# Optimization experiments

Hardware: AMD Instinct MI355X
Metric: run time of the kernel (lower is better)

## Reference

```python
import jax, jax.numpy as jnp
import numpy as np

T, B, I, H, NH = 256, 8, 1024, 1024, 16
DH = H // NH
LN_EPS = 1e-5


def setup_inputs() -> dict:
    key = jax.random.key(0)
    ks = jax.random.split(key, 8)
    def w(k, shape, fan_in):
        return jax.random.normal(k, shape, jnp.float32) / np.float32(np.sqrt(fan_in))
    inputs = jax.random.normal(ks[0], (T, B, I), jnp.float32)
    # 4 HybridGates (forget, input, update, output) stacked: Linear(I+H -> H)
    W_gates = w(ks[1], (4, H, I + H), I + H)
    b_gates = jnp.zeros((4, H), jnp.float32)
    ln_g = jnp.ones((4, H), jnp.float32)   # LayerNorm weight per gate
    ln_b = jnp.zeros((4, H), jnp.float32)  # LayerNorm bias per gate
    # MultiheadAttention in_proj (split into q/k/v) and out_proj
    Wq = w(ks[2], (H, H), H); Wk = w(ks[3], (H, H), H); Wv = w(ks[4], (H, H), H)
    bq = jnp.zeros((H,), jnp.float32); bk = jnp.zeros((H,), jnp.float32); bv = jnp.zeros((H,), jnp.float32)
    Wo = w(ks[5], (H, H), H); bo = jnp.zeros((H,), jnp.float32)
    return dict(inputs=inputs, W_gates=W_gates, b_gates=b_gates, ln_g=ln_g, ln_b=ln_b,
                Wq=Wq, Wk=Wk, Wv=Wv, bq=bq, bk=bk, bv=bv, Wo=Wo, bo=bo)


def _layernorm(x, g, b):
    m = jnp.mean(x, axis=-1, keepdims=True)
    v = jnp.var(x, axis=-1, keepdims=True)
    return (x - m) * jax.lax.rsqrt(v + LN_EPS) * g + b


def reference(inputs, W_gates, b_gates, ln_g, ln_b, Wq, Wk, Wv, bq, bk, bv, Wo, bo):
    Tn, Bn, _ = inputs.shape
    scale = 1.0 / np.float32(np.sqrt(DH))
    pos = jnp.arange(Tn)

    def step(carry, x_t):
        hx, cx, Kb, Vb, t = carry  # Kb/Vb: [T, B, NH, DH] cached projections of past outputs
        combined = jnp.concatenate([x_t, hx], axis=1)          # [B, I+H]
        z = jnp.einsum('bd,khd->kbh', combined, W_gates) + b_gates[:, None, :]
        z = _layernorm(z, ln_g[:, None, :], ln_b[:, None, :])  # [4, B, H]
        f = jax.nn.sigmoid(z[0]); i = jax.nn.sigmoid(z[1])
        g = jnp.tanh(z[2]);       o = jax.nn.sigmoid(z[3])
        cx = f * cx + i * g
        h0 = o * jnp.tanh(cx)                                   # [B, H]
        # attention of current hidden over all previously produced outputs
        q = (h0 @ Wq.T + bq).reshape(Bn, NH, DH)
        scores = jnp.einsum('bhd,sbhd->bhs', q, Kb) * scale     # [B, NH, T]
        scores = jnp.where((pos < t)[None, None, :], scores, -1e9)
        attn = jax.nn.softmax(scores, axis=-1)
        ctx = jnp.einsum('bhs,sbhd->bhd', attn, Vb).reshape(Bn, H)
        attn_out = ctx @ Wo.T + bo
        hx = h0 + jnp.where(t > 0, attn_out, 0.0)               # no attention at t=0
        # cache k/v projections of the new output (linear, so per-token projection is exact)
        Kb = Kb.at[t].set((hx @ Wk.T + bk).reshape(Bn, NH, DH))
        Vb = Vb.at[t].set((hx @ Wv.T + bv).reshape(Bn, NH, DH))
        return (hx, cx, Kb, Vb, t + 1), hx

    init = (jnp.zeros((Bn, H), inputs.dtype), jnp.zeros((Bn, H), inputs.dtype),
            jnp.zeros((Tn, Bn, NH, DH), inputs.dtype), jnp.zeros((Tn, Bn, NH, DH), inputs.dtype),
            jnp.int32(0))
    (hx, cx, _, _, _), outputs = jax.lax.scan(step, init, inputs)
    return outputs, hx, cx
```

## Files before the change

kernel.cpp:

```cpp
#include <hip/hip_runtime.h>
#include <math.h>

#define NBLK 256
#define NTHR 512
#define GATHER 255

#define OFF_HX    0
#define OFF_H0    8192
#define OFF_CTX   16384
#define OFF_Z     24576
#define OFF_KB    57344
#define OFF_VB    (OFF_KB + 2097152)
#define OFF_FLAGS (OFF_VB + 2097152)
#define FLG_U32   (4096 + 128)

#define S_WG    0
#define S_STAGE 32768
#define S_CX    36864
#define S_H0L   37888
#define S_Q     38912
#define S_PS    38976
#define S_RED   39232
#define S_R2    39248
#define S_EH    39264
#define S_ZX    39296
#define S_KVX   39424
#define LDS_FLOATS 39488
#define LDS_BYTES  (LDS_FLOATS * 4)

typedef unsigned long long u64;
union F2U { u64 u; float2 f; };

__device__ __forceinline__ float ld1(const float* p) {
    return __hip_atomic_load(const_cast<float*>(p), __ATOMIC_RELAXED, __HIP_MEMORY_SCOPE_AGENT);
}
__device__ __forceinline__ void st1(float* p, float v) {
    __hip_atomic_store(p, v, __ATOMIC_RELAXED, __HIP_MEMORY_SCOPE_AGENT);
}
__device__ __forceinline__ unsigned ldu(const unsigned* p) {
    return __hip_atomic_load(const_cast<unsigned*>(p), __ATOMIC_RELAXED, __HIP_MEMORY_SCOPE_AGENT);
}
__device__ __forceinline__ void stu(unsigned* p, unsigned v) {
    __hip_atomic_store(p, v, __ATOMIC_RELAXED, __HIP_MEMORY_SCOPE_AGENT);
}
__device__ __forceinline__ float2 ld2(const float* p) {
    F2U c; c.u = __hip_atomic_load(reinterpret_cast<u64*>(const_cast<float*>(p)),
                                   __ATOMIC_RELAXED, __HIP_MEMORY_SCOPE_AGENT);
    return c.f;
}
__device__ __forceinline__ float4 ld4(const float* p) {
    float2 a = ld2(p), b = ld2(p + 2);
    return make_float4(a.x, a.y, b.x, b.y);
}
__device__ __forceinline__ float dot4(const float4 a, const float4 b) {
    return a.x*b.x + a.y*b.y + a.z*b.z + a.w*b.w;
}

__device__ __forceinline__ void arrive(unsigned* flags, int blk, unsigned bc) {
    __syncthreads();
    if (threadIdx.x == 0) stu(flags + blk * 16, bc);
}
__device__ __forceinline__ void waitbar(unsigned* flags, unsigned* golines,
                                        unsigned bc, int blk) {
    if (blk == GATHER) {
        if (threadIdx.x < 256)
            while (ldu(flags + threadIdx.x * 16) < bc) __builtin_amdgcn_s_sleep(4);
        __syncthreads();
        if (threadIdx.x < 8) stu(golines + threadIdx.x * 16, bc);
    } else {
        if (threadIdx.x == 0)
            while (ldu(golines + (blk >> 5) * 16) < bc) __builtin_amdgcn_s_sleep(4);
    }
    __syncthreads();
}

__global__ __launch_bounds__(NTHR, 1)
void qlstm_kernel(const float* __restrict__ x,  const float* __restrict__ Wg,
                  const float* __restrict__ bg, const float* __restrict__ lng,
                  const float* __restrict__ lnb,const float* __restrict__ Wq,
                  const float* __restrict__ Wk, const float* __restrict__ Wv,
                  const float* __restrict__ bq, const float* __restrict__ bk,
                  const float* __restrict__ bv, const float* __restrict__ Wo,
                  const float* __restrict__ bo, float* __restrict__ out,
                  float* __restrict__ ws)
{
    extern __shared__ float lds[];
    const int blk = blockIdx.x, tid = threadIdx.x;
    const int w = tid >> 6, l = tid & 63;

    float* hx  = ws + OFF_HX;   float* h0g = ws + OFF_H0;
    float* ctx = ws + OFF_CTX;  float* z   = ws + OFF_Z;
    float* Kb  = ws + OFF_KB;   float* Vb  = ws + OFF_VB;
    unsigned* flags   = (unsigned*)(ws + OFF_FLAGS);
    unsigned* golines = flags + 4096;
    unsigned bc = 1;

    {
        const float* wsrc = Wg + (size_t)blk * 32768;
        #pragma unroll
        for (int j = 0; j < 16; ++j) {
            const int fi = j * 512 + tid;
            *(float4*)(lds + S_WG + fi * 4) = *(const float4*)(wsrc + fi * 4);
        }
    }
    const int kv_mat = blk >> 7;
    const int kv_h   = (blk & 127) * 8 + w;
    const float* kv_wrow = (kv_mat ? Wv : Wk) + (size_t)kv_h * 1024;
    float4 wkv[4];
    #pragma unroll
    for (int i = 0; i < 4; ++i) wkv[i] = *(const float4*)(kv_wrow + i * 256 + l * 4);
    const float kv_bias = (kv_mat ? bv : bk)[kv_h];
    const int g     = blk >> 6;
    const int hbase = (blk & 63) * 16;
    const int h0r   = hbase + 2 * w;
    const float bg0 = bg[g * 1024 + h0r], bg1 = bg[g * 1024 + h0r + 1];
    float lnw0[4], lnw1[4], lnb0[4], lnb1[4];
    #pragma unroll
    for (int g2 = 0; g2 < 4; ++g2) {
        lnw0[g2] = lng[g2 * 1024 + tid];       lnb0[g2] = lnb[g2 * 1024 + tid];
        lnw1[g2] = lng[g2 * 1024 + 512 + tid]; lnb1[g2] = lnb[g2 * 1024 + 512 + tid];
    }
    const float bo0 = bo[blk*4+0], bo1 = bo[blk*4+1], bo2 = bo[blk*4+2], bo3 = bo[blk*4+3];
    const int ab = blk >> 4, anh = blk & 15;
    const bool h0_writer = (blk < 128) && ((blk & 15) == 0);
    const int qdh = tid >> 3, qks = tid & 7;
    const float q_bias = (blk < 128) ? bq[anh * 64 + qdh] : 0.f;

    { const int gi = blk * NTHR + tid; if (gi < 8192) st1(hx + gi, 0.f); }
    if (tid < 256) *(float4*)(lds + S_CX + tid * 4) = make_float4(0,0,0,0);
    arrive(flags, blk, bc);

    for (int t = 0; t < 256; ++t) {
        float a0[8], a1[8];
        {
            const float* xt = x + (size_t)t * 8192;
            #pragma unroll
            for (int b = 0; b < 8; ++b) { a0[b] = 0.f; a1[b] = 0.f; }
            #pragma unroll
            for (int i = 0; i < 4; ++i) {
                const int k = i * 256 + l * 4;
                const float4 w0 = *(const float4*)(lds + S_WG + (2*w)   * 2048 + k);
                const float4 w1 = *(const float4*)(lds + S_WG + (2*w+1) * 2048 + k);
                #pragma unroll
                for (int b = 0; b < 8; ++b) {
                    const float4 a = *(const float4*)(xt + b * 1024 + k);
                    a0[b] += dot4(w0, a); a1[b] += dot4(w1, a);
                }
            }
        }
        waitbar(flags, golines, bc, blk);

        {
            float akv[8];
            #pragma unroll
            for (int b = 0; b < 8; ++b) akv[b] = 0.f;
            float2 hreg[8];
            #pragma unroll
            for (int c = 0; c < 2; ++c)
                #pragma unroll
                for (int j = 0; j < 4; ++j) {
                    const int idx = j * 512 + tid;
                    const int b = idx >> 8, off2 = idx & 255;
                    hreg[c * 4 + j] = ld2(hx + b * 1024 + c * 512 + off2 * 2);
                }
            #pragma unroll
            for (int c = 0; c < 2; ++c) {
                if (c) __syncthreads();
                #pragma unroll
                for (int j = 0; j < 4; ++j)
                    *(float2*)(lds + S_STAGE + (j * 512 + tid) * 2) = hreg[c * 4 + j];
                __syncthreads();
                #pragma unroll
                for (int ii = 0; ii < 2; ++ii) {
                    const int k = ii * 256 + l * 4;
                    const float4 w0 = *(const float4*)(lds + S_WG + (2*w)   * 2048 + 1024 + c * 512 + k);
                    const float4 w1 = *(const float4*)(lds + S_WG + (2*w+1) * 2048 + 1024 + c * 512 + k);
                    const float4 wk = wkv[c * 2 + ii];
                    #pragma unroll
                    for (int b = 0; b < 8; ++b) {
                        const float4 a = *(const float4*)(lds + S_STAGE + b * 512 + k);
                        a0[b] += dot4(w0, a); a1[b] += dot4(w1, a); akv[b] += dot4(wk, a);
                    }
                }
            }
            #pragma unroll
            for (int o = 1; o < 64; o <<= 1)
                #pragma unroll
                for (int b = 0; b < 8; ++b) {
                    a0[b]  += __shfl_xor(a0[b], o);
                    a1[b]  += __shfl_xor(a1[b], o);
                    akv[b] += __shfl_xor(akv[b], o);
                }
            if (l == 0) {
                #pragma unroll
                for (int b = 0; b < 8; ++b) {
                    lds[S_ZX + (2*w)   * 8 + b] = a0[b] + bg0;
                    lds[S_ZX + (2*w+1) * 8 + b] = a1[b] + bg1;
                    lds[S_KVX + w * 8 + b]      = akv[b] + kv_bias;
                }
            }
            __syncthreads();
            if (tid < 128) {
                const int h = tid & 15, b2 = tid >> 4;
                st1(z + (size_t)(g * 8 + b2) * 1024 + hbase + h, lds[S_ZX + h * 8 + b2]);
            } else if (tid < 192 && t > 0) {
                const int j = tid - 128;
                const int b2 = j >> 3, hh = j & 7;
                float* dst = kv_mat ? Vb : Kb;
                st1(dst + ((size_t)(t - 1) * 8 + b2) * 1024 + (blk & 127) * 8 + hh,
                    lds[S_KVX + hh * 8 + b2]);
            }
        }
        ++bc; arrive(flags, blk, bc);
        waitbar(flags, golines, bc, blk);

        if (blk < 128) {
            #pragma unroll
            for (int j = 0; j < 4; ++j) {
                const int idx = j * 512 + tid;
                const int g2 = idx >> 9, off2 = idx & 511;
                *(float2*)(lds + S_STAGE + idx * 2) = ld2(z + ((size_t)g2 * 8 + ab) * 1024 + off2 * 2);
            }
            __syncthreads();
            const int gt = w >> 1, hf = w & 1;
            float s = 0.f, q2s = 0.f;
            #pragma unroll
            for (int j = 0; j < 8; ++j) {
                const float v = lds[S_STAGE + gt * 1024 + hf * 512 + j * 64 + l];
                s += v; q2s += v * v;
            }
            #pragma unroll
            for (int o = 1; o < 64; o <<= 1) { s += __shfl_xor(s, o); q2s += __shfl_xor(q2s, o); }
            if (l == 0) { lds[S_RED + w] = s; lds[S_R2 + w] = q2s; }
            __syncthreads();
            float mean[4], rstd[4];
            #pragma unroll
            for (int g2 = 0; g2 < 4; ++g2) {
                const float ss = lds[S_RED + 2*g2] + lds[S_RED + 2*g2 + 1];
                const float qq = lds[S_R2  + 2*g2] + lds[S_R2  + 2*g2 + 1];
                const float m = ss * (1.f / 1024.f);
                mean[g2] = m;
                rstd[g2] = rsqrtf(qq * (1.f / 1024.f) - m * m + 1e-5f);
            }
            {
                float zv[4];
                #pragma unroll
                for (int g2 = 0; g2 < 4; ++g2)
                    zv[g2] = (lds[S_STAGE + g2 * 1024 + tid] - mean[g2]) * rstd[g2] * lnw0[g2] + lnb0[g2];
                const float f  = 1.f / (1.f + __expf(-zv[0]));
                const float ii = 1.f / (1.f + __expf(-zv[1]));
                const float gg = tanhf(zv[2]);
                const float oo = 1.f / (1.f + __expf(-zv[3]));
                const float c  = f * lds[S_CX + tid] + ii * gg;
                lds[S_CX + tid] = c;
                const float ho = oo * tanhf(c);
                lds[S_H0L + tid] = ho;
                if (h0_writer) st1(h0g + ab * 1024 + tid, ho);
            }
            {
                float zv[4];
                #pragma unroll
                for (int g2 = 0; g2 < 4; ++g2)
                    zv[g2] = (lds[S_STAGE + g2 * 1024 + 512 + tid] - mean[g2]) * rstd[g2] * lnw1[g2] + lnb1[g2];
                const float f  = 1.f / (1.f + __expf(-zv[0]));
                const float ii = 1.f / (1.f + __expf(-zv[1]));
                const float gg = tanhf(zv[2]);
                const float oo = 1.f / (1.f + __expf(-zv[3]));
                const float c  = f * lds[S_CX + 512 + tid] + ii * gg;
                lds[S_CX + 512 + tid] = c;
                const float ho = oo * tanhf(c);
                lds[S_H0L + 512 + tid] = ho;
                if (h0_writer) st1(h0g + ab * 1024 + 512 + tid, ho);
            }
            __syncthreads();
            {
                const float* wrow = Wq + (size_t)(anh * 64 + qdh) * 1024;
                float qa = 0.f;
                #pragma unroll 8
                for (int j = 0; j < 32; ++j) {
                    const int k = j * 32 + qks * 4;
                    qa += dot4(*(const float4*)(wrow + k), *(const float4*)(lds + S_H0L + k));
                }
                qa += __shfl_xor(qa, 1); qa += __shfl_xor(qa, 2); qa += __shfl_xor(qa, 4);
                if (qks == 0) lds[S_Q + qdh] = (qa + q_bias) * 0.125f;
            }
            __syncthreads();
            if (t > 0) {
                float sc = -1e30f;
                if (tid < t) {
                    const float* kr = Kb + ((size_t)tid * 8 + ab) * 1024 + anh * 64;
                    float d = 0.f;
                    #pragma unroll
                    for (int j = 0; j < 16; ++j) {
                        const float4 k4 = ld4(kr + j * 4);
                        d += k4.x*lds[S_Q + j*4]   + k4.y*lds[S_Q + j*4+1]
                           + k4.z*lds[S_Q + j*4+2] + k4.w*lds[S_Q + j*4+3];
                    }
                    sc = d;
                }
                float mx = sc;
                #pragma unroll
                for (int o = 1; o < 64; o <<= 1) mx = fmaxf(mx, __shfl_xor(mx, o));
                if (l == 0) lds[S_RED + w] = mx;
                __syncthreads();
                mx = lds[S_RED];
                #pragma unroll
                for (int j = 1; j < 8; ++j) mx = fmaxf(mx, lds[S_RED + j]);
                const float p = (tid < t) ? __expf(sc - mx) : 0.f;
                if (tid < 256) lds[S_PS + tid] = p;
                float ps = p;
                #pragma unroll
                for (int o = 1; o < 64; o <<= 1) ps += __shfl_xor(ps, o);
                if (l == 0) lds[S_R2 + w] = ps;
                __syncthreads();
                float tot = lds[S_R2];
                #pragma unroll
                for (int j = 1; j < 8; ++j) tot += lds[S_R2 + j];
                const float inv = 1.f / tot;
                const int dh2 = tid & 31, ss = tid >> 5;
                float cax = 0.f, cay = 0.f;
                for (int s2 = ss; s2 < t; s2 += 16) {
                    const float pp = lds[S_PS + s2];
                    const float2 v2 = ld2(Vb + ((size_t)s2 * 8 + ab) * 1024 + anh * 64 + dh2 * 2);
                    cax += pp * v2.x; cay += pp * v2.y;
                }
                *(float2*)(lds + S_STAGE + tid * 2) = make_float2(cax, cay);
                __syncthreads();
                if (tid < 64) {
                    float v = 0.f;
                    #pragma unroll
                    for (int j = 0; j < 16; ++j) v += lds[S_STAGE + j * 64 + tid];
                    st1(ctx + ab * 1024 + anh * 64 + tid, v * inv);
                }
            }
        }
        ++bc; arrive(flags, blk, bc);
        waitbar(flags, golines, bc, blk);

        {
            if (tid < 32)
                lds[S_EH + tid] = ld1(h0g + (size_t)(tid >> 2) * 1024 + blk * 4 + (tid & 3));
            const int b = w;
            float o0 = 0.f, o1 = 0.f, o2 = 0.f, o3 = 0.f;
            if (t > 0) {
                const float* cb = ctx + b * 1024;
                #pragma unroll
                for (int i = 0; i < 4; ++i) {
                    const int k = i * 256 + l * 4;
                    const float4 c4 = ld4(cb + k);
                    o0 += dot4(*(const float4*)(Wo + (size_t)(blk*4+0) * 1024 + k), c4);
                    o1 += dot4(*(const float4*)(Wo + (size_t)(blk*4+1) * 1024 + k), c4);
                    o2 += dot4(*(const float4*)(Wo + (size_t)(blk*4+2) * 1024 + k), c4);
                    o3 += dot4(*(const float4*)(Wo + (size_t)(blk*4+3) * 1024 + k), c4);
                }
                #pragma unroll
                for (int o = 1; o < 64; o <<= 1) {
                    o0 += __shfl_xor(o0, o); o1 += __shfl_xor(o1, o);
                    o2 += __shfl_xor(o2, o); o3 += __shfl_xor(o3, o);
                }
            }
            __syncthreads();
            if (l == 0) {
                const float v0 = (t > 0) ? lds[S_EH + w*4 + 0] + o0 + bo0 : lds[S_EH + w*4 + 0];
                const float v1 = (t > 0) ? lds[S_EH + w*4 + 1] + o1 + bo1 : lds[S_EH + w*4 + 1];
                const float v2 = (t > 0) ? lds[S_EH + w*4 + 2] + o2 + bo2 : lds[S_EH + w*4 + 2];
                const float v3 = (t > 0) ? lds[S_EH + w*4 + 3] + o3 + bo3 : lds[S_EH + w*4 + 3];
                st1(hx + b * 1024 + blk*4 + 0, v0);
                st1(hx + b * 1024 + blk*4 + 1, v1);
                st1(hx + b * 1024 + blk*4 + 2, v2);
                st1(hx + b * 1024 + blk*4 + 3, v3);
                float* op = out + (size_t)t * 8192 + b * 1024 + blk * 4;
                op[0] = v0; op[1] = v1; op[2] = v2; op[3] = v3;
            }
        }
        ++bc; arrive(flags, blk, bc);
    }
    waitbar(flags, golines, bc, blk);

    if (h0_writer) {
        out[2097152 + 8192 + ab * 1024 + tid]       = lds[S_CX + tid];
        out[2097152 + 8192 + ab * 1024 + 512 + tid] = lds[S_CX + 512 + tid];
    }
    if (blk >= 136 && blk < 144) {
        const int b = blk - 136;
        out[2097152 + b * 1024 + tid]       = ld1(hx + b * 1024 + tid);
        out[2097152 + b * 1024 + 512 + tid] = ld1(hx + b * 1024 + 512 + tid);
    }
}

extern "C" void kernel_launch(void* const* d_in, const int* in_sizes, int n_in,
                              void* d_out, int out_size, void* d_ws, size_t ws_size,
                              hipStream_t stream) {
    const float* x   = (const float*)d_in[0];
    const float* Wg  = (const float*)d_in[1];
    const float* bg  = (const float*)d_in[2];
    const float* lng = (const float*)d_in[3];
    const float* lnb = (const float*)d_in[4];
    const float* Wq  = (const float*)d_in[5];
    const float* Wk  = (const float*)d_in[6];
    const float* Wv  = (const float*)d_in[7];
    const float* bq  = (const float*)d_in[8];
    const float* bk  = (const float*)d_in[9];
    const float* bv  = (const float*)d_in[10];
    const float* Wo  = (const float*)d_in[11];
    const float* bo  = (const float*)d_in[12];
    float* out = (float*)d_out;
    float* ws  = (float*)d_ws;

    static int attr_set = 0;
    if (!attr_set) {
        hipFuncSetAttribute((const void*)qlstm_kernel,
                            hipFuncAttributeMaxDynamicSharedMemorySize, LDS_BYTES);
        attr_set = 1;
    }
    hipMemsetAsync((char*)d_ws + (size_t)OFF_FLAGS * 4, 0, (size_t)FLG_U32 * 4, stream);

    void* args[] = { &x, &Wg, &bg, &lng, &lnb, &Wq, &Wk, &Wv,
                     &bq, &bk, &bv, &Wo, &bo, &out, &ws };
    hipLaunchCooperativeKernel((void*)qlstm_kernel, dim3(NBLK), dim3(NTHR),
                               args, LDS_BYTES, stream);
}
```

Measured before the change: 11.72 ms.

## Store hidden state and K/V cache in bf16 and restructure score and out-proj mapping

Stores the broadcast hidden state and the K/V attention cache as packed bf16 instead of fp32. This halves the global traffic for the recurrent hidden-state reads and the attention cache scans. It also restructures the score computation so 16 lanes cooperate per key row with shuffle reductions, and remaps the out-projection so each block computes 2 rows by 2 batches. The cost is reduced precision in the recurrence and attention, which may push errors past tolerance, plus an extra barrier in the softmax.

```diff
diff --git a/kernel.cpp b/kernel.cpp
--- a/kernel.cpp
+++ b/kernel.cpp
@@ -6,12 +6,13 @@
 #define GATHER 255
 
 #define OFF_HX    0
-#define OFF_H0    8192
-#define OFF_CTX   16384
-#define OFF_Z     24576
-#define OFF_KB    57344
-#define OFF_VB    (OFF_KB + 2097152)
-#define OFF_FLAGS (OFF_VB + 2097152)
+#define OFF_HXH   8192
+#define OFF_H0    12288
+#define OFF_CTX   20480
+#define OFF_Z     28672
+#define OFF_KBH   61440
+#define OFF_VBH   (OFF_KBH + 1048576)
+#define OFF_FLAGS (OFF_VBH + 1048576)
 #define FLG_U32   (4096 + 128)
 
 #define S_WG    0
@@ -43,17 +44,37 @@
 __device__ __forceinline__ void stu(unsigned* p, unsigned v) {
     __hip_atomic_store(p, v, __ATOMIC_RELAXED, __HIP_MEMORY_SCOPE_AGENT);
 }
+__device__ __forceinline__ u64 ldu64(const unsigned* p) {
+    return __hip_atomic_load(reinterpret_cast<u64*>(const_cast<unsigned*>(p)),
+                             __ATOMIC_RELAXED, __HIP_MEMORY_SCOPE_AGENT);
+}
 __device__ __forceinline__ float2 ld2(const float* p) {
     F2U c; c.u = __hip_atomic_load(reinterpret_cast<u64*>(const_cast<float*>(p)),
                                    __ATOMIC_RELAXED, __HIP_MEMORY_SCOPE_AGENT);
     return c.f;
 }
+__device__ __forceinline__ void st2(float* p, float2 v) {
+    F2U c; c.f = v;
+    __hip_atomic_store(reinterpret_cast<u64*>(p), c.u,
+                       __ATOMIC_RELAXED, __HIP_MEMORY_SCOPE_AGENT);
+}
 __device__ __forceinline__ float4 ld4(const float* p) {
     float2 a = ld2(p), b = ld2(p + 2);
     return make_float4(a.x, a.y, b.x, b.y);
 }
 __device__ __forceinline__ float dot4(const float4 a, const float4 b) {
     return a.x*b.x + a.y*b.y + a.z*b.z + a.w*b.w;
+}
+__device__ __forceinline__ unsigned pack_bf16(float lo, float hi) {
+    unsigned ul = __builtin_bit_cast(unsigned, lo);
+    ul = (ul + 0x7FFFu + ((ul >> 16) & 1u)) >> 16;
+    unsigned uh = __builtin_bit_cast(unsigned, hi);
+    uh = (uh + 0x7FFFu + ((uh >> 16) & 1u)) >> 16;
+    return ul | (uh << 16);
+}
+__device__ __forceinline__ float2 unpack_bf16(unsigned u) {
+    return make_float2(__builtin_bit_cast(float, u << 16),
+                       __builtin_bit_cast(float, u & 0xFFFF0000u));
 }
 
 __device__ __forceinline__ void arrive(unsigned* flags, int blk, unsigned bc) {
@@ -88,9 +109,13 @@
     const int blk = blockIdx.x, tid = threadIdx.x;
     const int w = tid >> 6, l = tid & 63;
 
-    float* hx  = ws + OFF_HX;   float* h0g = ws + OFF_H0;
-    float* ctx = ws + OFF_CTX;  float* z   = ws + OFF_Z;
-    float* Kb  = ws + OFF_KB;   float* Vb  = ws + OFF_VB;
+    float* hx   = ws + OFF_HX;
+    unsigned* hxh = (unsigned*)(ws + OFF_HXH);
+    float* h0g  = ws + OFF_H0;
+    float* ctx  = ws + OFF_CTX;
+    float* z    = ws + OFF_Z;
+    unsigned* Kbh = (unsigned*)(ws + OFF_KBH);
+    unsigned* Vbh = (unsigned*)(ws + OFF_VBH);
     unsigned* flags   = (unsigned*)(ws + OFF_FLAGS);
     unsigned* golines = flags + 4096;
     unsigned bc = 1;
@@ -114,19 +139,27 @@
     const int hbase = (blk & 63) * 16;
     const int h0r   = hbase + 2 * w;
     const float bg0 = bg[g * 1024 + h0r], bg1 = bg[g * 1024 + h0r + 1];
-    float lnw0[4], lnw1[4], lnb0[4], lnb1[4];
+    float lnw0[4], lnw1[4], lnb0v[4], lnb1v[4];
     #pragma unroll
     for (int g2 = 0; g2 < 4; ++g2) {
-        lnw0[g2] = lng[g2 * 1024 + tid];       lnb0[g2] = lnb[g2 * 1024 + tid];
-        lnw1[g2] = lng[g2 * 1024 + 512 + tid]; lnb1[g2] = lnb[g2 * 1024 + 512 + tid];
-    }
-    const float bo0 = bo[blk*4+0], bo1 = bo[blk*4+1], bo2 = bo[blk*4+2], bo3 = bo[blk*4+3];
+        lnw0[g2] = lng[g2 * 1024 + tid];       lnb0v[g2] = lnb[g2 * 1024 + tid];
+        lnw1[g2] = lng[g2 * 1024 + 512 + tid]; lnb1v[g2] = lnb[g2 * 1024 + 512 + tid];
+    }
+    const int rg = blk >> 2, bp = blk & 3;
+    const int er0 = rg * 16 + 2 * w;
+    const int eb0 = bp * 2, eb1 = eb0 + 1;
+    const float bor0 = bo[er0], bor1 = bo[er0 + 1];
     const int ab = blk >> 4, anh = blk & 15;
     const bool h0_writer = (blk < 128) && ((blk & 15) == 0);
     const int qdh = tid >> 3, qks = tid & 7;
     const float q_bias = (blk < 128) ? bq[anh * 64 + qdh] : 0.f;
-
-    { const int gi = blk * NTHR + tid; if (gi < 8192) st1(hx + gi, 0.f); }
+    const int sr = tid >> 4, l16 = tid & 15;
+
+    {
+        const int gi = blk * NTHR + tid;
+        if (gi < 8192) st1(hx + gi, 0.f);
+        else if (gi < 12288) stu(hxh + gi - 8192, 0u);
+    }
     if (tid < 256) *(float4*)(lds + S_CX + tid * 4) = make_float4(0,0,0,0);
     arrive(flags, blk, bc);
 
@@ -154,21 +187,24 @@
             float akv[8];
             #pragma unroll
             for (int b = 0; b < 8; ++b) akv[b] = 0.f;
-            float2 hreg[8];
+            unsigned hregu[8];
             #pragma unroll
             for (int c = 0; c < 2; ++c)
                 #pragma unroll
                 for (int j = 0; j < 4; ++j) {
-                    const int idx = j * 512 + tid;
-                    const int b = idx >> 8, off2 = idx & 255;
-                    hreg[c * 4 + j] = ld2(hx + b * 1024 + c * 512 + off2 * 2);
+                    const int ix = j * 512 + tid;
+                    const int b = ix >> 8, p = ix & 255;
+                    hregu[c * 4 + j] = ldu(hxh + b * 512 + c * 256 + p);
                 }
             #pragma unroll
             for (int c = 0; c < 2; ++c) {
                 if (c) __syncthreads();
                 #pragma unroll
-                for (int j = 0; j < 4; ++j)
-                    *(float2*)(lds + S_STAGE + (j * 512 + tid) * 2) = hreg[c * 4 + j];
+                for (int j = 0; j < 4; ++j) {
+                    const int ix = j * 512 + tid;
+                    const int b = ix >> 8, p = ix & 255;
+                    *(float2*)(lds + S_STAGE + b * 512 + p * 2) = unpack_bf16(hregu[c * 4 + j]);
+                }
                 __syncthreads();
                 #pragma unroll
                 for (int ii = 0; ii < 2; ++ii) {
@@ -203,12 +239,12 @@
             if (tid < 128) {
                 const int h = tid & 15, b2 = tid >> 4;
                 st1(z + (size_t)(g * 8 + b2) * 1024 + hbase + h, lds[S_ZX + h * 8 + b2]);
-            } else if (tid < 192 && t > 0) {
+            } else if (tid < 160 && t > 0) {
                 const int j = tid - 128;
-                const int b2 = j >> 3, hh = j & 7;
-                float* dst = kv_mat ? Vb : Kb;
-                st1(dst + ((size_t)(t - 1) * 8 + b2) * 1024 + (blk & 127) * 8 + hh,
-                    lds[S_KVX + hh * 8 + b2]);
+                const int b2 = j >> 2, hp = j & 3;
+                unsigned* dst = kv_mat ? Vbh : Kbh;
+                stu(dst + ((size_t)(t - 1) * 8 + b2) * 512 + (blk & 127) * 4 + hp,
+                    pack_bf16(lds[S_KVX + (2*hp) * 8 + b2], lds[S_KVX + (2*hp+1) * 8 + b2]));
             }
         }
         ++bc; arrive(flags, blk, bc);
@@ -246,7 +282,7 @@
                 float zv[4];
                 #pragma unroll
                 for (int g2 = 0; g2 < 4; ++g2)
-                    zv[g2] = (lds[S_STAGE + g2 * 1024 + tid] - mean[g2]) * rstd[g2] * lnw0[g2] + lnb0[g2];
+                    zv[g2] = (lds[S_STAGE + g2 * 1024 + tid] - mean[g2]) * rstd[g2] * lnw0[g2] + lnb0v[g2];
                 const float f  = 1.f / (1.f + __expf(-zv[0]));
                 const float ii = 1.f / (1.f + __expf(-zv[1]));
                 const float gg = tanhf(zv[2]);
@@ -261,7 +297,7 @@
                 float zv[4];
                 #pragma unroll
                 for (int g2 = 0; g2 < 4; ++g2)
-                    zv[g2] = (lds[S_STAGE + g2 * 1024 + 512 + tid] - mean[g2]) * rstd[g2] * lnw1[g2] + lnb1[g2];
+                    zv[g2] = (lds[S_STAGE + g2 * 1024 + 512 + tid] - mean[g2]) * rstd[g2] * lnw1[g2] + lnb1v[g2];
                 const float f  = 1.f / (1.f + __expf(-zv[0]));
                 const float ii = 1.f / (1.f + __expf(-zv[1]));
                 const float gg = tanhf(zv[2]);
@@ -286,18 +322,22 @@
             }
             __syncthreads();
             if (t > 0) {
-                float sc = -1e30f;
-                if (tid < t) {
-                    const float* kr = Kb + ((size_t)tid * 8 + ab) * 1024 + anh * 64;
+                for (int s0 = 0; s0 < t; s0 += 32) {
+                    const int s2 = s0 + sr;
                     float d = 0.f;
-                    #pragma unroll
-                    for (int j = 0; j < 16; ++j) {
-                        const float4 k4 = ld4(kr + j * 4);
-                        d += k4.x*lds[S_Q + j*4]   + k4.y*lds[S_Q + j*4+1]
-                           + k4.z*lds[S_Q + j*4+2] + k4.w*lds[S_Q + j*4+3];
+                    if (s2 < t) {
+                        F2U c; c.u = ldu64(Kbh + ((size_t)s2 * 8 + ab) * 512 + anh * 32 + l16 * 2);
+                        const float2 p0 = unpack_bf16((unsigned)(c.u & 0xFFFFFFFFu));
+                        const float2 p1 = unpack_bf16((unsigned)(c.u >> 32));
+                        d = p0.x*lds[S_Q + l16*4]   + p0.y*lds[S_Q + l16*4+1]
+                          + p1.x*lds[S_Q + l16*4+2] + p1.y*lds[S_Q + l16*4+3];
                     }
-                    sc = d;
-                }
+                    d += __shfl_xor(d, 1); d += __shfl_xor(d, 2);
+                    d += __shfl_xor(d, 4); d += __shfl_xor(d, 8);
+                    if (s2 < t && l16 == 0) lds[S_PS + s2] = d;
+                }
+                __syncthreads();
+                float sc = (tid < t) ? lds[S_PS + tid] : -1e30f;
                 float mx = sc;
                 #pragma unroll
                 for (int o = 1; o < 64; o <<= 1) mx = fmaxf(mx, __shfl_xor(mx, o));
@@ -307,6 +347,7 @@
                 #pragma unroll
                 for (int j = 1; j < 8; ++j) mx = fmaxf(mx, lds[S_RED + j]);
                 const float p = (tid < t) ? __expf(sc - mx) : 0.f;
+                __syncthreads();
                 if (tid < 256) lds[S_PS + tid] = p;
                 float ps = p;
                 #pragma unroll
@@ -317,11 +358,11 @@
                 #pragma unroll
                 for (int j = 1; j < 8; ++j) tot += lds[S_R2 + j];
                 const float inv = 1.f / tot;
-                const int dh2 = tid & 31, ss = tid >> 5;
+                const int dh2 = tid & 31, ss2 = tid >> 5;
                 float cax = 0.f, cay = 0.f;
-                for (int s2 = ss; s2 < t; s2 += 16) {
+                for (int s2 = ss2; s2 < t; s2 += 16) {
                     const float pp = lds[S_PS + s2];
-                    const float2 v2 = ld2(Vb + ((size_t)s2 * 8 + ab) * 1024 + anh * 64 + dh2 * 2);
+                    const float2 v2 = unpack_bf16(ldu(Vbh + ((size_t)s2 * 8 + ab) * 512 + anh * 32 + dh2));
                     cax += pp * v2.x; cay += pp * v2.y;
                 }
                 *(float2*)(lds + S_STAGE + tid * 2) = make_float2(cax, cay);
@@ -338,39 +379,45 @@
         waitbar(flags, golines, bc, blk);
 
         {
-            if (tid < 32)
-                lds[S_EH + tid] = ld1(h0g + (size_t)(tid >> 2) * 1024 + blk * 4 + (tid & 3));
-            const int b = w;
-            float o0 = 0.f, o1 = 0.f, o2 = 0.f, o3 = 0.f;
+            if (tid < 16) {
+                const int bsel = tid >> 3, hp = tid & 7;
+                *(float2*)(lds + S_EH + bsel * 16 + hp * 2) =
+                    ld2(h0g + (size_t)(eb0 + bsel) * 1024 + rg * 16 + hp * 2);
+            }
+            float o00 = 0.f, o01 = 0.f, o10 = 0.f, o11 = 0.f;
             if (t > 0) {
-                const float* cb = ctx + b * 1024;
                 #pragma unroll
                 for (int i = 0; i < 4; ++i) {
                     const int k = i * 256 + l * 4;
-                    const float4 c4 = ld4(cb + k);
-                    o0 += dot4(*(const float4*)(Wo + (size_t)(blk*4+0) * 1024 + k), c4);
-                    o1 += dot4(*(const float4*)(Wo + (size_t)(blk*4+1) * 1024 + k), c4);
-                    o2 += dot4(*(const float4*)(Wo + (size_t)(blk*4+2) * 1024 + k), c4);
-                    o3 += dot4(*(const float4*)(Wo + (size_t)(blk*4+3) * 1024 + k), c4);
+                    const float4 c0 = ld4(ctx + (size_t)eb0 * 1024 + k);
+                    const float4 c1 = ld4(ctx + (size_t)eb1 * 1024 + k);
+                    const float4 w0 = *(const float4*)(Wo + (size_t)er0 * 1024 + k);
+                    const float4 w1 = *(const float4*)(Wo + (size_t)(er0+1) * 1024 + k);
+                    o00 += dot4(w0, c0); o01 += dot4(w0, c1);
+                    o10 += dot4(w1, c0); o11 += dot4(w1, c1);
                 }
                 #pragma unroll
                 for (int o = 1; o < 64; o <<= 1) {
-                    o0 += __shfl_xor(o0, o); o1 += __shfl_xor(o1, o);
-                    o2 += __shfl_xor(o2, o); o3 += __shfl_xor(o3, o);
+                    o00 += __shfl_xor(o00, o); o01 += __shfl_xor(o01, o);
+                    o10 += __shfl_xor(o10, o); o11 += __shfl_xor(o11, o);
                 }
             }
             __syncthreads();
             if (l == 0) {
-                const float v0 = (t > 0) ? lds[S_EH + w*4 + 0] + o0 + bo0 : lds[S_EH + w*4 + 0];
-                const float v1 = (t > 0) ? lds[S_EH + w*4 + 1] + o1 + bo1 : lds[S_EH + w*4 + 1];
-                const float v2 = (t > 0) ? lds[S_EH + w*4 + 2] + o2 + bo2 : lds[S_EH + w*4 + 2];
-                const float v3 = (t > 0) ? lds[S_EH + w*4 + 3] + o3 + bo3 : lds[S_EH + w*4 + 3];
-                st1(hx + b * 1024 + blk*4 + 0, v0);
-                st1(hx + b * 1024 + blk*4 + 1, v1);
-                st1(hx + b * 1024 + blk*4 + 2, v2);
-                st1(hx + b * 1024 + blk*4 + 3, v3);
-                float* op = out + (size_t)t * 8192 + b * 1024 + blk * 4;
-                op[0] = v0; op[1] = v1; op[2] = v2; op[3] = v3;
+                const float h00 = lds[S_EH + 2*w],      h10 = lds[S_EH + 2*w + 1];
+                const float h01 = lds[S_EH + 16 + 2*w], h11 = lds[S_EH + 16 + 2*w + 1];
+                const float v00 = (t > 0) ? h00 + o00 + bor0 : h00;
+                const float v10 = (t > 0) ? h10 + o10 + bor1 : h10;
+                const float v01 = (t > 0) ? h01 + o01 + bor0 : h01;
+                const float v11 = (t > 0) ? h11 + o11 + bor1 : h11;
+                *(float2*)(out + (size_t)t * 8192 + eb0 * 1024 + er0) = make_float2(v00, v10);
+                *(float2*)(out + (size_t)t * 8192 + eb1 * 1024 + er0) = make_float2(v01, v11);
+                stu(hxh + eb0 * 512 + (er0 >> 1), pack_bf16(v00, v10));
+                stu(hxh + eb1 * 512 + (er0 >> 1), pack_bf16(v01, v11));
+                if (t == 255) {
+                    st2(hx + eb0 * 1024 + er0, make_float2(v00, v10));
+                    st2(hx + eb1 * 1024 + er0, make_float2(v01, v11));
+                }
             }
         }
         ++bc; arrive(flags, blk, bc);
```

Result: slower. 12.72 ms (+8.6%).

## Replace global barrier before out-projection with per-batch completion flags

Applied to the files above, without the earlier changes.

Removes the grid-wide barrier between the attention/context phase and the output-projection phase. Each attention block now publishes a per-block completion flag, and each output block waits only on the 32 attention blocks of the two batch rows it needs. The out-projection work is redistributed so each block computes 2 rows for 2 batches. The V accumulation loop is also unrolled with multiple accumulators, and the z loads are batched into registers before the LDS stores. This trades a full barrier for finer-grained flag polling and extra flag memory, and the flag ordering relies on relaxed atomics.

```diff
diff --git a/kernel.cpp b/kernel.cpp
--- a/kernel.cpp
+++ b/kernel.cpp
@@ -12,7 +12,7 @@
 #define OFF_KB    57344
 #define OFF_VB    (OFF_KB + 2097152)
 #define OFF_FLAGS (OFF_VB + 2097152)
-#define FLG_U32   (4096 + 128)
+#define FLG_U32   (4096 + 128 + 2048)
 
 #define S_WG    0
 #define S_STAGE 32768
@@ -48,6 +48,11 @@
                                    __ATOMIC_RELAXED, __HIP_MEMORY_SCOPE_AGENT);
     return c.f;
 }
+__device__ __forceinline__ void st2(float* p, float2 v) {
+    F2U c; c.f = v;
+    __hip_atomic_store(reinterpret_cast<u64*>(p), c.u,
+                       __ATOMIC_RELAXED, __HIP_MEMORY_SCOPE_AGENT);
+}
 __device__ __forceinline__ float4 ld4(const float* p) {
     float2 a = ld2(p), b = ld2(p + 2);
     return make_float4(a.x, a.y, b.x, b.y);
@@ -93,6 +98,7 @@
     float* Kb  = ws + OFF_KB;   float* Vb  = ws + OFF_VB;
     unsigned* flags   = (unsigned*)(ws + OFF_FLAGS);
     unsigned* golines = flags + 4096;
+    unsigned* cflg    = golines + 128;
     unsigned bc = 1;
 
     {
@@ -114,13 +120,16 @@
     const int hbase = (blk & 63) * 16;
     const int h0r   = hbase + 2 * w;
     const float bg0 = bg[g * 1024 + h0r], bg1 = bg[g * 1024 + h0r + 1];
-    float lnw0[4], lnw1[4], lnb0[4], lnb1[4];
+    float lnw0[4], lnw1[4], lnb0v[4], lnb1v[4];
     #pragma unroll
     for (int g2 = 0; g2 < 4; ++g2) {
-        lnw0[g2] = lng[g2 * 1024 + tid];       lnb0[g2] = lnb[g2 * 1024 + tid];
-        lnw1[g2] = lng[g2 * 1024 + 512 + tid]; lnb1[g2] = lnb[g2 * 1024 + 512 + tid];
-    }
-    const float bo0 = bo[blk*4+0], bo1 = bo[blk*4+1], bo2 = bo[blk*4+2], bo3 = bo[blk*4+3];
+        lnw0[g2] = lng[g2 * 1024 + tid];       lnb0v[g2] = lnb[g2 * 1024 + tid];
+        lnw1[g2] = lng[g2 * 1024 + 512 + tid]; lnb1v[g2] = lnb[g2 * 1024 + 512 + tid];
+    }
+    const int rg = blk >> 2, bp = blk & 3;
+    const int er0 = rg * 16 + 2 * w;
+    const int eb0 = bp * 2, eb1 = eb0 + 1;
+    const float bor0 = bo[er0], bor1 = bo[er0 + 1];
     const int ab = blk >> 4, anh = blk & 15;
     const bool h0_writer = (blk < 128) && ((blk & 15) == 0);
     const int qdh = tid >> 3, qks = tid & 7;
@@ -215,11 +224,17 @@
         waitbar(flags, golines, bc, blk);
 
         if (blk < 128) {
-            #pragma unroll
-            for (int j = 0; j < 4; ++j) {
-                const int idx = j * 512 + tid;
-                const int g2 = idx >> 9, off2 = idx & 511;
-                *(float2*)(lds + S_STAGE + idx * 2) = ld2(z + ((size_t)g2 * 8 + ab) * 1024 + off2 * 2);
+            {
+                float2 zreg[4];
+                #pragma unroll
+                for (int j = 0; j < 4; ++j) {
+                    const int idx = j * 512 + tid;
+                    const int g2 = idx >> 9, off2 = idx & 511;
+                    zreg[j] = ld2(z + ((size_t)g2 * 8 + ab) * 1024 + off2 * 2);
+                }
+                #pragma unroll
+                for (int j = 0; j < 4; ++j)
+                    *(float2*)(lds + S_STAGE + (j * 512 + tid) * 2) = zreg[j];
             }
             __syncthreads();
             const int gt = w >> 1, hf = w & 1;
@@ -246,7 +261,7 @@
                 float zv[4];
                 #pragma unroll
                 for (int g2 = 0; g2 < 4; ++g2)
-                    zv[g2] = (lds[S_STAGE + g2 * 1024 + tid] - mean[g2]) * rstd[g2] * lnw0[g2] + lnb0[g2];
+                    zv[g2] = (lds[S_STAGE + g2 * 1024 + tid] - mean[g2]) * rstd[g2] * lnw0[g2] + lnb0v[g2];
                 const float f  = 1.f / (1.f + __expf(-zv[0]));
                 const float ii = 1.f / (1.f + __expf(-zv[1]));
                 const float gg = tanhf(zv[2]);
@@ -261,7 +276,7 @@
                 float zv[4];
                 #pragma unroll
                 for (int g2 = 0; g2 < 4; ++g2)
-                    zv[g2] = (lds[S_STAGE + g2 * 1024 + 512 + tid] - mean[g2]) * rstd[g2] * lnw1[g2] + lnb1[g2];
+                    zv[g2] = (lds[S_STAGE + g2 * 1024 + 512 + tid] - mean[g2]) * rstd[g2] * lnw1[g2] + lnb1v[g2];
                 const float f  = 1.f / (1.f + __expf(-zv[0]));
                 const float ii = 1.f / (1.f + __expf(-zv[1]));
                 const float gg = tanhf(zv[2]);
@@ -317,14 +332,28 @@
                 #pragma unroll
                 for (int j = 1; j < 8; ++j) tot += lds[S_R2 + j];
                 const float inv = 1.f / tot;
-                const int dh2 = tid & 31, ss = tid >> 5;
-                float cax = 0.f, cay = 0.f;
-                for (int s2 = ss; s2 < t; s2 += 16) {
+                const int dh2 = tid & 31, ss2 = tid >> 5;
+                const float* vbase = Vb + (size_t)ab * 1024 + anh * 64 + dh2 * 2;
+                float cax0 = 0.f, cay0 = 0.f, cax1 = 0.f, cay1 = 0.f;
+                int s2 = ss2;
+                for (; s2 + 48 < t; s2 += 64) {
+                    const float2 va = ld2(vbase + (size_t)(s2)      * 8192);
+                    const float2 vb = ld2(vbase + (size_t)(s2 + 16) * 8192);
+                    const float2 vc = ld2(vbase + (size_t)(s2 + 32) * 8192);
+                    const float2 vd = ld2(vbase + (size_t)(s2 + 48) * 8192);
+                    const float pa = lds[S_PS + s2],      pb = lds[S_PS + s2 + 16];
+                    const float pc = lds[S_PS + s2 + 32], pd = lds[S_PS + s2 + 48];
+                    cax0 += pa * va.x; cay0 += pa * va.y;
+                    cax1 += pb * vb.x; cay1 += pb * vb.y;
+                    cax0 += pc * vc.x; cay0 += pc * vc.y;
+                    cax1 += pd * vd.x; cay1 += pd * vd.y;
+                }
+                for (; s2 < t; s2 += 16) {
                     const float pp = lds[S_PS + s2];
-                    const float2 v2 = ld2(Vb + ((size_t)s2 * 8 + ab) * 1024 + anh * 64 + dh2 * 2);
-                    cax += pp * v2.x; cay += pp * v2.y;
-                }
-                *(float2*)(lds + S_STAGE + tid * 2) = make_float2(cax, cay);
+                    const float2 v2 = ld2(vbase + (size_t)s2 * 8192);
+                    cax0 += pp * v2.x; cay0 += pp * v2.y;
+                }
+                *(float2*)(lds + S_STAGE + tid * 2) = make_float2(cax0 + cax1, cay0 + cay1);
                 __syncthreads();
                 if (tid < 64) {
                     float v = 0.f;
@@ -333,44 +362,60 @@
                     st1(ctx + ab * 1024 + anh * 64 + tid, v * inv);
                 }
             }
-        }
-        ++bc; arrive(flags, blk, bc);
-        waitbar(flags, golines, bc, blk);
+            __syncthreads();
+            if (tid == 0) stu(cflg + blk * 16, (unsigned)(t + 1));
+        }
 
         {
-            if (tid < 32)
-                lds[S_EH + tid] = ld1(h0g + (size_t)(tid >> 2) * 1024 + blk * 4 + (tid & 3));
-            const int b = w;
-            float o0 = 0.f, o1 = 0.f, o2 = 0.f, o3 = 0.f;
+            if (tid < 32) {
+                const int pb = (tid < 16) ? eb0 : eb1;
+                const unsigned* f = cflg + (pb * 16 + (tid & 15)) * 16;
+                while (ldu(f) < (unsigned)(t + 1)) __builtin_amdgcn_s_sleep(2);
+            }
+            __syncthreads();
+        }
+
+        {
+            if (tid < 16) {
+                const int bsel = tid >> 3, hp = tid & 7;
+                *(float2*)(lds + S_EH + bsel * 16 + hp * 2) =
+                    ld2(h0g + (size_t)(eb0 + bsel) * 1024 + rg * 16 + hp * 2);
+            }
+            float o00 = 0.f, o01 = 0.f, o10 = 0.f, o11 = 0.f;
             if (t > 0) {
-                const float* cb = ctx + b * 1024;
+                float4 c0r[4], c1r[4];
                 #pragma unroll
                 for (int i = 0; i < 4; ++i) {
                     const int k = i * 256 + l * 4;
-                    const float4 c4 = ld4(cb + k);
-                    o0 += dot4(*(const float4*)(Wo + (size_t)(blk*4+0) * 1024 + k), c4);
-                    o1 += dot4(*(const float4*)(Wo + (size_t)(blk*4+1) * 1024 + k), c4);
-                    o2 += dot4(*(const float4*)(Wo + (size_t)(blk*4+2) * 1024 + k), c4);
-                    o3 += dot4(*(const float4*)(Wo + (size_t)(blk*4+3) * 1024 + k), c4);
+                    c0r[i] = ld4(ctx + (size_t)eb0 * 1024 + k);
+                    c1r[i] = ld4(ctx + (size_t)eb1 * 1024 + k);
+                }
+                #pragma unroll
+                for (int i = 0; i < 4; ++i) {
+                    const int k = i * 256 + l * 4;
+                    const float4 w0 = *(const float4*)(Wo + (size_t)er0 * 1024 + k);
+                    const float4 w1 = *(const float4*)(Wo + (size_t)(er0+1) * 1024 + k);
+                    o00 += dot4(w0, c0r[i]); o01 += dot4(w0, c1r[i]);
+                    o10 += dot4(w1, c0r[i]); o11 += dot4(w1, c1r[i]);
                 }
                 #pragma unroll
                 for (int o = 1; o < 64; o <<= 1) {
-                    o0 += __shfl_xor(o0, o); o1 += __shfl_xor(o1, o);
-                    o2 += __shfl_xor(o2, o); o3 += __shfl_xor(o3, o);
+                    o00 += __shfl_xor(o00, o); o01 += __shfl_xor(o01, o);
+                    o10 += __shfl_xor(o10, o); o11 += __shfl_xor(o11, o);
                 }
             }
             __syncthreads();
             if (l == 0) {
-                const float v0 = (t > 0) ? lds[S_EH + w*4 + 0] + o0 + bo0 : lds[S_EH + w*4 + 0];
-                const float v1 = (t > 0) ? lds[S_EH + w*4 + 1] + o1 + bo1 : lds[S_EH + w*4 + 1];
-                const float v2 = (t > 0) ? lds[S_EH + w*4 + 2] + o2 + bo2 : lds[S_EH + w*4 + 2];
-                const float v3 = (t > 0) ? lds[S_EH + w*4 + 3] + o3 + bo3 : lds[S_EH + w*4 + 3];
-                st1(hx + b * 1024 + blk*4 + 0, v0);
-                st1(hx + b * 1024 + blk*4 + 1, v1);
-                st1(hx + b * 1024 + blk*4 + 2, v2);
-                st1(hx + b * 1024 + blk*4 + 3, v3);
-                float* op = out + (size_t)t * 8192 + b * 1024 + blk * 4;
-                op[0] = v0; op[1] = v1; op[2] = v2; op[3] = v3;
+                const float h00 = lds[S_EH + 2*w],      h10 = lds[S_EH + 2*w + 1];
+                const float h01 = lds[S_EH + 16 + 2*w], h11 = lds[S_EH + 16 + 2*w + 1];
+                const float v00 = (t > 0) ? h00 + o00 + bor0 : h00;
+                const float v10 = (t > 0) ? h10 + o10 + bor1 : h10;
+                const float v01 = (t > 0) ? h01 + o01 + bor0 : h01;
+                const float v11 = (t > 0) ? h11 + o11 + bor1 : h11;
+                st2(hx + eb0 * 1024 + er0, make_float2(v00, v10));
+                st2(hx + eb1 * 1024 + er0, make_float2(v01, v11));
+                *(float2*)(out + (size_t)t * 8192 + eb0 * 1024 + er0) = make_float2(v00, v10);
+                *(float2*)(out + (size_t)t * 8192 + eb1 * 1024 + er0) = make_float2(v01, v11);
             }
         }
         ++bc; arrive(flags, blk, bc);
```

After: 10.28 ms. 1.14x faster.
